# Kernel optimization log

Hardware: AMD Instinct MI355X
Metric: run time of the kernel (lower is better)

## Reference

```python
import jax, jax.numpy as jnp
import numpy as np

NM = 16  # n_modes


def setup_inputs() -> dict:
    key = jax.random.key(0)
    k1, k2, k3, k4 = jax.random.split(key, 4)
    B, M, N, I, O = 8, 256, 256, 64, 64
    std = 1.0 / (I * O)
    x = jax.random.normal(k1, (B, M, N, I), dtype=jnp.float32)
    w1 = jax.random.normal(k2, (I, O, NM, NM, 2), dtype=jnp.float32) * std
    w2 = jax.random.normal(k3, (I, O, NM, NM, 2), dtype=jnp.float32) * std
    lin_w = jax.random.normal(k4, (O, O), dtype=jnp.float32) * (1.0 / np.sqrt(O))
    lin_b = jnp.zeros((O,), dtype=jnp.float32)
    return {"x": x, "w1": w1, "w2": w2, "lin_w": lin_w, "lin_b": lin_b}


def _to_complex(w):
    return jax.lax.complex(w[..., 0], w[..., 1])


def reference(x, w1, w2, lin_w, lin_b):
    B, M, N, I = x.shape
    O = w1.shape[1]
    # [B, I, M, N]
    xt = jnp.transpose(x, (0, 3, 1, 2))
    # rfft over last two dims -> [B, I, M, N//2 + 1] complex
    x_ft = jnp.fft.rfft2(xt, s=(M, N), axes=(-2, -1))
    w1c = _to_complex(w1)  # [I, O, NM, NM]
    w2c = _to_complex(w2)
    # truncated complex matmuls over low modes (top rows) and high-negative modes (bottom rows)
    out_top = jnp.einsum('bixy,ioxy->boxy', x_ft[:, :, :NM, :NM], w1c)
    out_bot = jnp.einsum('bixy,ioxy->boxy', x_ft[:, :, -NM:, :NM], w2c)
    zeros_mid = jnp.zeros((B, O, M - 2 * NM, NM), dtype=out_top.dtype)
    rows = jnp.concatenate([out_top, zeros_mid, out_bot], axis=2)  # [B, O, M, NM]
    zeros_right = jnp.zeros((B, O, M, N // 2 + 1 - NM), dtype=out_top.dtype)
    out_ft = jnp.concatenate([rows, zeros_right], axis=3)  # [B, O, M, N//2+1]
    y = jnp.fft.irfft2(out_ft, s=(M, N), axes=(-2, -1))  # real [B, O, M, N]
    y = jnp.transpose(y, (0, 2, 3, 1))  # [B, M, N, O]
    res = y @ lin_w + lin_b
    return jax.nn.relu(y + res)
```

## Files before the change

### kernel.cpp

```cpp
#include <hip/hip_runtime.h>
#include <hip/hip_bf16.h>
#include <math.h>


#define TOFF  65536
#define XOFF  (TOFF + 4194304)
#define YOFF  (XOFF + 524288)
#define GOFF  (YOFF + 524288)

__global__ __launch_bounds__(256) void setup_tables(const float* __restrict__ lin_w,
                                                    float* __restrict__ ws) {
    int j = blockIdx.x * 256 + threadIdx.x;
    const float ANG = 0.024543692606170259f;
    if (j < 4096) {
        int n = j >> 4, ky = j & 15;
        int a = (n * ky) & 255;
        float s, c; sincosf(ANG * (float)a, &s, &c);
        float* p = ws + n * 32 + ky * 2;
        p[0] = c; p[1] = -s;
    } else if (j < 12288) {
        int e = j - 4096; int m = e >> 5, kx = e & 31;
        int kxe = kx + (kx < 16 ? 0 : 224);
        int a = (m * kxe) & 255;
        float s, c; sincosf(ANG * (float)a, &s, &c);
        int g = kx >> 2, kl = kx & 3;
        float* p = ws + 8192 + g * 2048 + m * 8 + kl * 2;
        p[0] = c; p[1] = -s;
    } else if (j < 20480) {
        int e = j - 12288; int kx = e >> 8, m = e & 255;
        int kxe = kx + (kx < 16 ? 0 : 224);
        int a = (kxe * m) & 255;
        float s, c; sincosf(ANG * (float)a, &s, &c);
        float* p = ws + 24576 + (kx * 256 + m) * 2;
        p[0] = c * (1.0f / 256.0f);
        p[1] = s * (1.0f / 256.0f);
    } else if (j < 28672) {
        int e = j - 20480; int f = e >> 8, n = e & 255;
        int ky = f >> 1, h = f & 1;
        int a = (ky * n) & 255;
        float s, c; sincosf(ANG * (float)a, &s, &c);
        float scale = (ky == 0 ? 1.0f : 2.0f) * (1.0f / 256.0f);
        ws[40960 + f * 256 + n] = h ? (-scale * s) : (scale * c);
    } else if (j < 32768) {
        int e = j - 28672;
        int op = e >> 6, o = e & 63;
        ws[49152 + e] = lin_w[e] + ((op == o) ? 1.0f : 0.0f);
    }
}

__global__ __launch_bounds__(256) void stageA(const float* __restrict__ x,
                                              const float* __restrict__ tabA,
                                              float* __restrict__ T) {
    __shared__ float red[4 * 16 * 64 * 2];
    int bid = blockIdx.x;
    int b = bid >> 8, m = bid & 255;
    int t = threadIdx.x;
    int i = t & 63, w = t >> 6;
    const float* xp = x + (size_t)bid * 16384 + (size_t)w * 4096 + i;
    float accR[16], accI[16];
#pragma unroll
    for (int k = 0; k < 16; ++k) { accR[k] = 0.f; accI[k] = 0.f; }
    int tw0 = __builtin_amdgcn_readfirstlane(w * 64 * 32);
#pragma unroll 4
    for (int nn = 0; nn < 64; ++nn) {
        float xv = xp[nn * 64];
        const float* tp = tabA + tw0 + nn * 32;
#pragma unroll
        for (int k = 0; k < 16; ++k) {
            accR[k] = fmaf(tp[2 * k], xv, accR[k]);
            accI[k] = fmaf(tp[2 * k + 1], xv, accI[k]);
        }
    }
#pragma unroll
    for (int k = 0; k < 16; ++k) {
        red[(w * 16 + k) * 128 + i * 2]     = accR[k];
        red[(w * 16 + k) * 128 + i * 2 + 1] = accI[k];
    }
    __syncthreads();
    int ky = t >> 4, i0 = (t & 15) * 4;
    float4 s0 = make_float4(0, 0, 0, 0), s1 = make_float4(0, 0, 0, 0);
#pragma unroll
    for (int ww = 0; ww < 4; ++ww) {
        const float* rp = red + (ww * 16 + ky) * 128 + i0 * 2;
        float4 a = *(const float4*)rp;
        float4 bq = *(const float4*)(rp + 4);
        s0.x += a.x; s0.y += a.y; s0.z += a.z; s0.w += a.w;
        s1.x += bq.x; s1.y += bq.y; s1.z += bq.z; s1.w += bq.w;
    }
    float* Tf = T + (((size_t)(b * 16 + ky) * 256 + m) * 64 + i0) * 2;
    *(float4*)Tf = s0;
    *(float4*)(Tf + 4) = s1;
}

__global__ __launch_bounds__(256) void stageB(const float* __restrict__ T,
                                              const float* __restrict__ twF,
                                              float* __restrict__ X) {
    int bid = blockIdx.x;
    int b = bid >> 5;
    int ky = (bid >> 1) & 15;
    int half = bid & 1;
    int t = threadIdx.x, i = t & 63, kg = t >> 6;
    int g = half * 4 + kg;
    const float2* Tp = (const float2*)T + (size_t)(b * 16 + ky) * 256 * 64 + i;
    const float* tw = twF + __builtin_amdgcn_readfirstlane(g * 2048);
    float r0 = 0, r1 = 0, r2 = 0, r3 = 0;
    float q0 = 0, q1 = 0, q2 = 0, q3 = 0;
#pragma unroll 4
    for (int m = 0; m < 256; ++m) {
        float2 tv = Tp[(size_t)m * 64];
        const float* tp = tw + m * 8;
        r0 = fmaf(tv.x, tp[0], fmaf(-tv.y, tp[1], r0));
        q0 = fmaf(tv.x, tp[1], fmaf( tv.y, tp[0], q0));
        r1 = fmaf(tv.x, tp[2], fmaf(-tv.y, tp[3], r1));
        q1 = fmaf(tv.x, tp[3], fmaf( tv.y, tp[2], q1));
        r2 = fmaf(tv.x, tp[4], fmaf(-tv.y, tp[5], r2));
        q2 = fmaf(tv.x, tp[5], fmaf( tv.y, tp[4], q2));
        r3 = fmaf(tv.x, tp[6], fmaf(-tv.y, tp[7], r3));
        q3 = fmaf(tv.x, tp[7], fmaf( tv.y, tp[6], q3));
    }
    int kx0 = g * 4;
    float2* Xb = (float2*)X;
    size_t base = ((size_t)(b * 16 + ky) * 32 + kx0) * 64 + i;
    Xb[base + 0 * 64] = make_float2(r0, q0);
    Xb[base + 1 * 64] = make_float2(r1, q1);
    Xb[base + 2 * 64] = make_float2(r2, q2);
    Xb[base + 3 * 64] = make_float2(r3, q3);
}

__global__ __launch_bounds__(256) void stageC(const float* __restrict__ Xg,
                                              const float* __restrict__ w1,
                                              const float* __restrict__ w2,
                                              const float* __restrict__ Wf,
                                              float* __restrict__ Y2) {
    __shared__ float Ws[64 * 64 * 2];
    __shared__ float Xs[8 * 64 * 2];
    __shared__ float Ys[8 * 64 * 2];
    __shared__ float Wfs[64 * 64];
    int bid = blockIdx.x;
    int kx = bid & 31, ky = bid >> 5;
    int t = threadIdx.x;
    const float* wsrc = (kx < 16) ? w1 : w2;
    int xx = kx & 15;
#pragma unroll
    for (int q = 0; q < 16; ++q) {
        int p = t + q * 256;
        int ii = p >> 6, oo = p & 63;
        float2 wv = *(const float2*)(wsrc + ((size_t)(ii * 64 + oo) * 256 + xx * 16 + ky) * 2);
        ((float2*)Ws)[ii * 64 + oo] = wv;
    }
#pragma unroll
    for (int q = 0; q < 2; ++q) {
        int p = t + q * 256;
        int bb = p >> 6, ii = p & 63;
        ((float2*)Xs)[bb * 64 + ii] =
            ((const float2*)Xg)[((size_t)(bb * 16 + ky) * 32 + kx) * 64 + ii];
    }
#pragma unroll
    for (int q = 0; q < 16; ++q) Wfs[t + q * 256] = Wf[t + q * 256];
    __syncthreads();
    int o = t & 63, bg = t >> 6;
    float yr0 = 0, yi0 = 0, yr1 = 0, yi1 = 0;
    for (int ii = 0; ii < 64; ++ii) {
        float2 w = ((float2*)Ws)[ii * 64 + o];
        float2 xa = ((float2*)Xs)[bg * 64 + ii];
        float2 xb = ((float2*)Xs)[(bg + 4) * 64 + ii];
        yr0 = fmaf(xa.x, w.x, fmaf(-xa.y, w.y, yr0));
        yi0 = fmaf(xa.x, w.y, fmaf( xa.y, w.x, yi0));
        yr1 = fmaf(xb.x, w.x, fmaf(-xb.y, w.y, yr1));
        yi1 = fmaf(xb.x, w.y, fmaf( xb.y, w.x, yi1));
    }
    ((float2*)Ys)[bg * 64 + o] = make_float2(yr0, yi0);
    ((float2*)Ys)[(bg + 4) * 64 + o] = make_float2(yr1, yi1);
    __syncthreads();
    float zr0 = 0, zi0 = 0, zr1 = 0, zi1 = 0;
    for (int op = 0; op < 64; ++op) {
        float wf = Wfs[op * 64 + o];
        float2 ya = ((float2*)Ys)[bg * 64 + op];
        float2 yb = ((float2*)Ys)[(bg + 4) * 64 + op];
        zr0 = fmaf(ya.x, wf, zr0); zi0 = fmaf(ya.y, wf, zi0);
        zr1 = fmaf(yb.x, wf, zr1); zi1 = fmaf(yb.y, wf, zi1);
    }
    float2* Yb = (float2*)Y2;
    Yb[((size_t)(bg * 32 + kx) * 16 + ky) * 64 + o] = make_float2(zr0, zi0);
    Yb[((size_t)((bg + 4) * 32 + kx) * 16 + ky) * 64 + o] = make_float2(zr1, zi1);
}

__global__ __launch_bounds__(512) void stageD(const float* __restrict__ Y2,
                                              const float* __restrict__ twI,
                                              float* __restrict__ G) {
    __shared__ float Ysl[16 * 64 * 2];
    int bid = blockIdx.x;
    int b = bid >> 5, mg = bid & 31;
    int t = threadIdx.x, o = t & 63, ml = t >> 6;
    int m = mg * 8 + ml;
    float gr[16], gi[16];
#pragma unroll
    for (int k = 0; k < 16; ++k) { gr[k] = 0.f; gi[k] = 0.f; }
    for (int kx = 0; kx < 32; ++kx) {
        __syncthreads();
        const float2* src = (const float2*)Y2 + (size_t)(b * 32 + kx) * 1024;
#pragma unroll
        for (int q = 0; q < 2; ++q) ((float2*)Ysl)[t + q * 512] = src[t + q * 512];
        __syncthreads();
        int off = __builtin_amdgcn_readfirstlane((kx * 256 + m) * 2);
        float c = twI[off], d = twI[off + 1];
#pragma unroll
        for (int ky = 0; ky < 16; ++ky) {
            float2 yv = ((float2*)Ysl)[ky * 64 + o];
            gr[ky] = fmaf(yv.x, c, fmaf(-yv.y, d, gr[ky]));
            gi[ky] = fmaf(yv.x, d, fmaf( yv.y, c, gi[ky]));
        }
    }
    float2* Gb = (float2*)G;
#pragma unroll
    for (int ky = 0; ky < 16; ++ky)
        Gb[((size_t)(b * 256 + m) * 16 + ky) * 64 + o] = make_float2(gr[ky], gi[ky]);
}

__global__ __launch_bounds__(256) void stageE(const float* __restrict__ G,
                                              const float* __restrict__ tabE,
                                              const float* __restrict__ lin_b,
                                              float* __restrict__ out) {
    __shared__ float Bs[32 * 256];
    __shared__ float Hs[32 * 64];
    int bid = blockIdx.x;
    int t = threadIdx.x;
    const float4* tE4 = (const float4*)tabE;
#pragma unroll
    for (int q = 0; q < 8; ++q) ((float4*)Bs)[t + q * 256] = tE4[t + q * 256];
    const float2* Gp = (const float2*)G + (size_t)bid * 1024;
#pragma unroll
    for (int q = 0; q < 4; ++q) {
        int p = t + q * 256;
        int ky = p >> 6, o = p & 63;
        float2 g = Gp[p];
        Hs[(2 * ky) * 64 + o] = g.x;
        Hs[(2 * ky + 1) * 64 + o] = g.y;
    }
    __syncthreads();
    int o4 = (t & 15) * 4, n0 = (t >> 4) * 16;
    float acc[16][4];
#pragma unroll
    for (int j = 0; j < 16; ++j) { acc[j][0] = acc[j][1] = acc[j][2] = acc[j][3] = 0.f; }
    for (int f = 0; f < 32; ++f) {
        float4 h = *(const float4*)(Hs + f * 64 + o4);
        const float* bp = Bs + f * 256 + n0;
        float4 a0 = *(const float4*)(bp);
        float4 a1 = *(const float4*)(bp + 4);
        float4 a2 = *(const float4*)(bp + 8);
        float4 a3 = *(const float4*)(bp + 12);
        float av[16] = {a0.x, a0.y, a0.z, a0.w, a1.x, a1.y, a1.z, a1.w,
                        a2.x, a2.y, a2.z, a2.w, a3.x, a3.y, a3.z, a3.w};
#pragma unroll
        for (int j = 0; j < 16; ++j) {
            acc[j][0] = fmaf(av[j], h.x, acc[j][0]);
            acc[j][1] = fmaf(av[j], h.y, acc[j][1]);
            acc[j][2] = fmaf(av[j], h.z, acc[j][2]);
            acc[j][3] = fmaf(av[j], h.w, acc[j][3]);
        }
    }
    float4 bias = *(const float4*)(lin_b + o4);
    float* outp = out + (size_t)bid * 256 * 64;
#pragma unroll
    for (int j = 0; j < 16; ++j) {
        int n = n0 + j;
        float4 r;
        r.x = fmaxf(acc[j][0] + bias.x, 0.f);
        r.y = fmaxf(acc[j][1] + bias.y, 0.f);
        r.z = fmaxf(acc[j][2] + bias.z, 0.f);
        r.w = fmaxf(acc[j][3] + bias.w, 0.f);
        *(float4*)(outp + (size_t)n * 64 + o4) = r;
    }
}

extern "C" void kernel_launch(void* const* d_in, const int* in_sizes, int n_in,
                              void* d_out, int out_size, void* d_ws, size_t ws_size,
                              hipStream_t stream) {
    const float* x     = (const float*)d_in[0];
    const float* w1    = (const float*)d_in[1];
    const float* w2    = (const float*)d_in[2];
    const float* lin_w = (const float*)d_in[3];
    const float* lin_b = (const float*)d_in[4];
    float* ws  = (float*)d_ws;
    float* out = (float*)d_out;

    float* T  = ws + TOFF;
    float* X  = ws + XOFF;
    float* Y2 = ws + YOFF;
    float* G  = ws + GOFF;

    setup_tables<<<128, 256, 0, stream>>>(lin_w, ws);
    stageA<<<2048, 256, 0, stream>>>(x, ws, T);
    stageB<<<256, 256, 0, stream>>>(T, ws + 8192, X);
    stageC<<<512, 256, 0, stream>>>(X, w1, w2, ws + 49152, Y2);
    stageD<<<256, 512, 0, stream>>>(Y2, ws + 24576, G);
    stageE<<<2048, 256, 0, stream>>>(G, ws + 40960, lin_b, out);
}
```

Baseline: 155.0 us.

## Stage x rows in LDS for stageA and split stageB's m-loop across waves

StageA now copies each 256x64 slab of x into LDS with direct global-to-LDS loads in two chunks. Each wave then computes 4 ky modes over all 256 n, instead of 16 modes over a quarter of n followed by a shared-memory reduction. The twiddle table is re-laid out per wave to match. StageB doubles its block size to 512 threads, splits the 256-long m reduction between two halves and combines them through LDS, which raises parallelism in that latency-bound stage. The cost is more LDS traffic and extra syncs in stageA, and each thread in stageA does four times the loop iterations.

```diff
diff --git a/kernel.cpp b/kernel.cpp
--- a/kernel.cpp
+++ b/kernel.cpp
@@ -16,7 +16,8 @@
         int n = j >> 4, ky = j & 15;
         int a = (n * ky) & 255;
         float s, c; sincosf(ANG * (float)a, &s, &c);
-        float* p = ws + n * 32 + ky * 2;
+        int w = ky >> 2, jj = ky & 3;
+        float* p = ws + w * 2048 + n * 8 + jj * 2;
         p[0] = c; p[1] = -s;
     } else if (j < 12288) {
         int e = j - 4096; int m = e >> 5, kx = e & 31;
@@ -51,80 +52,102 @@
 __global__ __launch_bounds__(256) void stageA(const float* __restrict__ x,
                                               const float* __restrict__ tabA,
                                               float* __restrict__ T) {
-    __shared__ float red[4 * 16 * 64 * 2];
+    __shared__ float xs[8192];
     int bid = blockIdx.x;
     int b = bid >> 8, m = bid & 255;
     int t = threadIdx.x;
     int i = t & 63, w = t >> 6;
-    const float* xp = x + (size_t)bid * 16384 + (size_t)w * 4096 + i;
-    float accR[16], accI[16];
-#pragma unroll
-    for (int k = 0; k < 16; ++k) { accR[k] = 0.f; accI[k] = 0.f; }
-    int tw0 = __builtin_amdgcn_readfirstlane(w * 64 * 32);
+    int lane = i;
+    const float* twp = tabA + __builtin_amdgcn_readfirstlane(w * 2048);
+    float aR[4], aI[4];
+#pragma unroll
+    for (int j = 0; j < 4; ++j) { aR[j] = 0.f; aI[j] = 0.f; }
+    const float* xbase = x + (size_t)bid * 16384;
+#pragma unroll
+    for (int c = 0; c < 2; ++c) {
+        if (c) __syncthreads();
+        {
+            const float* gsrc = xbase + c * 8192 + (w * 8) * 256 + lane * 4;
+            float* ldst = xs + (w * 8) * 256;
+#pragma unroll
+            for (int q = 0; q < 8; ++q) {
+                __builtin_amdgcn_global_load_lds(
+                    (const __attribute__((address_space(1))) void*)(gsrc + q * 256),
+                    (__attribute__((address_space(3))) void*)(uintptr_t)(ldst + q * 256),
+                    16, 0, 0);
+            }
+        }
+        asm volatile("s_waitcnt vmcnt(0)" ::: "memory");
+        __syncthreads();
+        const float* tc = twp + c * 1024;
 #pragma unroll 4
-    for (int nn = 0; nn < 64; ++nn) {
-        float xv = xp[nn * 64];
-        const float* tp = tabA + tw0 + nn * 32;
-#pragma unroll
-        for (int k = 0; k < 16; ++k) {
-            accR[k] = fmaf(tp[2 * k], xv, accR[k]);
-            accI[k] = fmaf(tp[2 * k + 1], xv, accI[k]);
+        for (int nn = 0; nn < 128; ++nn) {
+            float xv = xs[nn * 64 + i];
+            const float* tp = tc + nn * 8;
+            aR[0] = fmaf(tp[0], xv, aR[0]); aI[0] = fmaf(tp[1], xv, aI[0]);
+            aR[1] = fmaf(tp[2], xv, aR[1]); aI[1] = fmaf(tp[3], xv, aI[1]);
+            aR[2] = fmaf(tp[4], xv, aR[2]); aI[2] = fmaf(tp[5], xv, aI[2]);
+            aR[3] = fmaf(tp[6], xv, aR[3]); aI[3] = fmaf(tp[7], xv, aI[3]);
         }
     }
-#pragma unroll
-    for (int k = 0; k < 16; ++k) {
-        red[(w * 16 + k) * 128 + i * 2]     = accR[k];
-        red[(w * 16 + k) * 128 + i * 2 + 1] = accI[k];
-    }
-    __syncthreads();
-    int ky = t >> 4, i0 = (t & 15) * 4;
-    float4 s0 = make_float4(0, 0, 0, 0), s1 = make_float4(0, 0, 0, 0);
-#pragma unroll
-    for (int ww = 0; ww < 4; ++ww) {
-        const float* rp = red + (ww * 16 + ky) * 128 + i0 * 2;
-        float4 a = *(const float4*)rp;
-        float4 bq = *(const float4*)(rp + 4);
-        s0.x += a.x; s0.y += a.y; s0.z += a.z; s0.w += a.w;
-        s1.x += bq.x; s1.y += bq.y; s1.z += bq.z; s1.w += bq.w;
-    }
-    float* Tf = T + (((size_t)(b * 16 + ky) * 256 + m) * 64 + i0) * 2;
-    *(float4*)Tf = s0;
-    *(float4*)(Tf + 4) = s1;
-}
-
-__global__ __launch_bounds__(256) void stageB(const float* __restrict__ T,
+    float2* Tb = (float2*)T;
+#pragma unroll
+    for (int j = 0; j < 4; ++j) {
+        int ky = w * 4 + j;
+        Tb[((size_t)(b * 16 + ky) * 256 + m) * 64 + i] = make_float2(aR[j], aI[j]);
+    }
+}
+
+__global__ __launch_bounds__(512) void stageB(const float* __restrict__ T,
                                               const float* __restrict__ twF,
                                               float* __restrict__ X) {
+    __shared__ float red[4 * 4 * 64 * 2];
     int bid = blockIdx.x;
     int b = bid >> 5;
     int ky = (bid >> 1) & 15;
     int half = bid & 1;
-    int t = threadIdx.x, i = t & 63, kg = t >> 6;
-    int g = half * 4 + kg;
+    int t = threadIdx.x, i = t & 63;
+    int q = (t >> 6) & 3, h = t >> 8;
+    int Q = half * 4 + q;
     const float2* Tp = (const float2*)T + (size_t)(b * 16 + ky) * 256 * 64 + i;
-    const float* tw = twF + __builtin_amdgcn_readfirstlane(g * 2048);
+    const float* tw = twF + __builtin_amdgcn_readfirstlane(Q * 2048);
     float r0 = 0, r1 = 0, r2 = 0, r3 = 0;
-    float q0 = 0, q1 = 0, q2 = 0, q3 = 0;
+    float s0 = 0, s1 = 0, s2 = 0, s3 = 0;
+    int m0 = h * 128;
 #pragma unroll 4
-    for (int m = 0; m < 256; ++m) {
+    for (int mm = 0; mm < 128; ++mm) {
+        int m = m0 + mm;
         float2 tv = Tp[(size_t)m * 64];
         const float* tp = tw + m * 8;
         r0 = fmaf(tv.x, tp[0], fmaf(-tv.y, tp[1], r0));
-        q0 = fmaf(tv.x, tp[1], fmaf( tv.y, tp[0], q0));
+        s0 = fmaf(tv.x, tp[1], fmaf( tv.y, tp[0], s0));
         r1 = fmaf(tv.x, tp[2], fmaf(-tv.y, tp[3], r1));
-        q1 = fmaf(tv.x, tp[3], fmaf( tv.y, tp[2], q1));
+        s1 = fmaf(tv.x, tp[3], fmaf( tv.y, tp[2], s1));
         r2 = fmaf(tv.x, tp[4], fmaf(-tv.y, tp[5], r2));
-        q2 = fmaf(tv.x, tp[5], fmaf( tv.y, tp[4], q2));
+        s2 = fmaf(tv.x, tp[5], fmaf( tv.y, tp[4], s2));
         r3 = fmaf(tv.x, tp[6], fmaf(-tv.y, tp[7], r3));
-        q3 = fmaf(tv.x, tp[7], fmaf( tv.y, tp[6], q3));
-    }
-    int kx0 = g * 4;
-    float2* Xb = (float2*)X;
-    size_t base = ((size_t)(b * 16 + ky) * 32 + kx0) * 64 + i;
-    Xb[base + 0 * 64] = make_float2(r0, q0);
-    Xb[base + 1 * 64] = make_float2(r1, q1);
-    Xb[base + 2 * 64] = make_float2(r2, q2);
-    Xb[base + 3 * 64] = make_float2(r3, q3);
+        s3 = fmaf(tv.x, tp[7], fmaf( tv.y, tp[6], s3));
+    }
+    float2* rp = (float2*)red + (q * 4) * 64 + i;
+    if (h == 1) {
+        rp[0 * 64] = make_float2(r0, s0);
+        rp[1 * 64] = make_float2(r1, s1);
+        rp[2 * 64] = make_float2(r2, s2);
+        rp[3 * 64] = make_float2(r3, s3);
+    }
+    __syncthreads();
+    if (h == 0) {
+        float2 p0 = rp[0 * 64], p1 = rp[1 * 64], p2 = rp[2 * 64], p3 = rp[3 * 64];
+        r0 += p0.x; s0 += p0.y; r1 += p1.x; s1 += p1.y;
+        r2 += p2.x; s2 += p2.y; r3 += p3.x; s3 += p3.y;
+        int kx0 = Q * 4;
+        float2* Xb = (float2*)X;
+        size_t base = ((size_t)(b * 16 + ky) * 32 + kx0) * 64 + i;
+        Xb[base + 0 * 64] = make_float2(r0, s0);
+        Xb[base + 1 * 64] = make_float2(r1, s1);
+        Xb[base + 2 * 64] = make_float2(r2, s2);
+        Xb[base + 3 * 64] = make_float2(r3, s3);
+    }
 }
 
 __global__ __launch_bounds__(256) void stageC(const float* __restrict__ Xg,
@@ -200,7 +223,7 @@
         __syncthreads();
         const float2* src = (const float2*)Y2 + (size_t)(b * 32 + kx) * 1024;
 #pragma unroll
-        for (int q = 0; q < 2; ++q) ((float2*)Ysl)[t + q * 512] = src[t + q * 512];
+        for (int qq = 0; qq < 2; ++qq) ((float2*)Ysl)[t + qq * 512] = src[t + qq * 512];
         __syncthreads();
         int off = __builtin_amdgcn_readfirstlane((kx * 256 + m) * 2);
         float c = twI[off], d = twI[off + 1];
@@ -291,7 +314,7 @@
 
     setup_tables<<<128, 256, 0, stream>>>(lin_w, ws);
     stageA<<<2048, 256, 0, stream>>>(x, ws, T);
-    stageB<<<256, 256, 0, stream>>>(T, ws + 8192, X);
+    stageB<<<256, 512, 0, stream>>>(T, ws + 8192, X);
     stageC<<<512, 256, 0, stream>>>(X, w1, w2, ws + 49152, Y2);
     stageD<<<256, 512, 0, stream>>>(Y2, ws + 24576, G);
     stageE<<<2048, 256, 0, stream>>>(G, ws + 40960, lin_b, out);
```

Measured after the change: 178.9 us. 15.5% more time.
